# Optimization experiments

Hardware: AMD Instinct MI355X
Metric: run time of the kernel (lower is better)

Reference implementation:

```python
import jax, jax.numpy as jnp
import numpy as np

TEMPERATURE = 0.5
EPS = 1e-12  # matches torch F.normalize eps


def _l2_normalize(x):
    norm = jnp.linalg.norm(x, axis=-1, keepdims=True)
    return x / jnp.maximum(norm, EPS)


def setup_inputs() -> dict:
    key = jax.random.key(0)
    k1, k2, k3 = jax.random.split(key, 3)
    N, D = 16384, 128
    self_predictions = jax.random.normal(k1, (N, D), dtype=jnp.float32)
    pos_predictions = jax.random.normal(k2, (N, D), dtype=jnp.float32)
    labels1 = jax.random.randint(k3, (N,), 0, 100, dtype=jnp.int64)
    return {
        "self_predictions": self_predictions,
        "pos_predictions": pos_predictions,
        "labels1": labels1,
    }


def reference(self_predictions, pos_predictions, labels1):
    N = labels1.shape[0]
    a = _l2_normalize(self_predictions)  # [N, D]
    b = _l2_normalize(pos_predictions)   # [N, D]
    # cosine similarity of already-normalized rows == dot product (GEMM form)
    sim = jnp.einsum("nd,md->nm", a, b)  # [N, N]
    neg_mask = (labels1[:, None] != labels1[None, :]).astype(sim.dtype)  # 1 - mask
    neg = jnp.exp(-sim / TEMPERATURE) * neg_mask
    return neg.sum() / (N * (N - 1))
```

## Files before the change

kernel.cpp:

```cpp
#include <hip/hip_runtime.h>

typedef unsigned char u8;
typedef unsigned short u16;
typedef float f32x4 __attribute__((ext_vector_type(4)));
typedef int i32x4 __attribute__((ext_vector_type(4)));
typedef int i32x8 __attribute__((ext_vector_type(8)));

#define NROWS 16384
#define DIM 128

#define NEG2LOG2E -2.8853900817779268f
#define SCALE ((float)(1.0 / (16384.0 * 16383.0)))

#define SCALE1 0x7F7F7F7F

#define KMAX 320
#define NCORR 100
#define NGEMM 4096

__global__ __launch_bounds__(256) void norm_kernel(
    const float* __restrict__ a, const float* __restrict__ b,
    u8* __restrict__ aO, u8* __restrict__ bO)
{
    int tid  = threadIdx.x;
    int lane = tid & 63;
    int w    = tid >> 6;
    int half = lane >> 5;
    int l32  = lane & 31;
    long row = (long)blockIdx.x * 8 + w * 2 + half;

    const float4 va = ((const float4*)(a + row * DIM))[l32];
    float sa = va.x * va.x + va.y * va.y + va.z * va.z + va.w * va.w;
    #pragma unroll
    for (int off = 16; off; off >>= 1) sa += __shfl_xor(sa, off, 64);
    float inva = 1.0f / fmaxf(sqrtf(sa), 1e-12f);
    int pa = __builtin_amdgcn_cvt_pk_fp8_f32(va.x * inva, va.y * inva, 0, false);
    pa = __builtin_amdgcn_cvt_pk_fp8_f32(va.z * inva, va.w * inva, pa, true);
    ((int*)(aO + row * DIM))[l32] = pa;

    const float4 vb = ((const float4*)(b + row * DIM))[l32];
    float sb = vb.x * vb.x + vb.y * vb.y + vb.z * vb.z + vb.w * vb.w;
    #pragma unroll
    for (int off = 16; off; off >>= 1) sb += __shfl_xor(sb, off, 64);
    float invb = NEG2LOG2E / fmaxf(sqrtf(sb), 1e-12f);
    int pb = __builtin_amdgcn_cvt_pk_fp8_f32(vb.x * invb, vb.y * invb, 0, false);
    pb = __builtin_amdgcn_cvt_pk_fp8_f32(vb.z * invb, vb.w * invb, pb, true);
    ((int*)(bO + row * DIM))[l32] = pb;
}

__global__ __launch_bounds__(256, 3) void gemm_kernel(
    const u8* __restrict__ A, const u8* __restrict__ B,
    const int* __restrict__ labels,
    float* __restrict__ partials, float* __restrict__ corrP)
{
    __shared__ u8 sStage[4][2][4096];
    __shared__ int sIdx[KMAX];
    __shared__ float redS[4];
    __shared__ int sCnt;

    int tid  = threadIdx.x;
    int lane = tid & 63;
    int w    = tid >> 6;
    int mrow = lane & 15;
    int q    = lane >> 4;

    if (blockIdx.x < NCORR) {
        int l = blockIdx.x;
        if (tid == 0) sCnt = 0;
        __syncthreads();

        for (int i = tid; i < NROWS; i += 256)
            if (labels[i] == l) {
                int p = atomicAdd(&sCnt, 1);
                if (p < KMAX) sIdx[p] = i;
            }
        __syncthreads();

        int k = sCnt < KMAX ? sCnt : KMAX;
        int nt = (k + 15) >> 4;
        int ntk = nt << 4;
        for (int r = k + tid; r < ntk; r += 256) sIdx[r] = sIdx[0];
        __syncthreads();

        int npairs = nt * nt;
        float s = 0.0f;
        for (int tp = w; tp < npairs; tp += 8) {
            int tpB = tp + 4;
            bool has2 = tpB < npairs;
            int tp2 = has2 ? tpB : tp;

            int ti1 = tp / nt,  tj1 = tp  - ti1 * nt;
            int ti2 = tp2 / nt, tj2 = tp2 - ti2 * nt;
            int ri1 = sIdx[ti1 * 16 + mrow], rj1 = sIdx[tj1 * 16 + mrow];
            int ri2 = sIdx[ti2 * 16 + mrow], rj2 = sIdx[tj2 * 16 + mrow];

            const u8* pa1 = A + (size_t)ri1 * DIM + q * 32;
            const u8* pb1 = B + (size_t)rj1 * DIM + q * 32;
            const u8* pa2 = A + (size_t)ri2 * DIM + q * 32;
            const u8* pb2 = B + (size_t)rj2 * DIM + q * 32;

            i32x8 aF1, bF1, aF2, bF2;
            *((i32x4*)&aF1)     = *(const i32x4*)pa1;
            *((i32x4*)&aF1 + 1) = *(const i32x4*)(pa1 + 16);
            *((i32x4*)&bF1)     = *(const i32x4*)pb1;
            *((i32x4*)&bF1 + 1) = *(const i32x4*)(pb1 + 16);
            *((i32x4*)&aF2)     = *(const i32x4*)pa2;
            *((i32x4*)&aF2 + 1) = *(const i32x4*)(pa2 + 16);
            *((i32x4*)&bF2)     = *(const i32x4*)pb2;
            *((i32x4*)&bF2 + 1) = *(const i32x4*)(pb2 + 16);

            f32x4 acc1 = (f32x4){0.f, 0.f, 0.f, 0.f};
            f32x4 acc2 = (f32x4){0.f, 0.f, 0.f, 0.f};
            acc1 = __builtin_amdgcn_mfma_scale_f32_16x16x128_f8f6f4(
                aF1, bF1, acc1, 0, 0, 0, SCALE1, 0, SCALE1);
            acc2 = __builtin_amdgcn_mfma_scale_f32_16x16x128_f8f6f4(
                aF2, bF2, acc2, 0, 0, 0, SCALE1, 0, SCALE1);

            int i1 = ti1 * 16 + q * 4, j1 = tj1 * 16 + mrow;
            int i2 = ti2 * 16 + q * 4, j2 = tj2 * 16 + mrow;
            #pragma unroll
            for (int r = 0; r < 4; r++) {
                float e1 = __builtin_amdgcn_exp2f(acc1[r]);
                s += ((i1 + r) < k && j1 < k) ? e1 : 0.0f;
                float e2 = __builtin_amdgcn_exp2f(acc2[r]);
                s += (has2 && (i2 + r) < k && j2 < k) ? e2 : 0.0f;
            }
        }

        #pragma unroll
        for (int off = 32; off; off >>= 1) s += __shfl_xor(s, off, 64);
        if (lane == 0) redS[w] = s;
        __syncthreads();
        if (tid == 0)
            corrP[l] = (redS[0] + redS[1] + redS[2] + redS[3]) * SCALE;
        return;
    }

    int g  = blockIdx.x - NCORR;
    int r0 = (g & 255) * 64;
    int c0 = (g >> 8) * 1024 + w * 256;

    i32x8 a8[4];
    #pragma unroll
    for (int mi = 0; mi < 4; mi++) {
        const u8* pa = A + (size_t)(r0 + mi * 16 + mrow) * DIM + q * 32;
        *((i32x4*)&a8[mi])     = *(const i32x4*)pa;
        *((i32x4*)&a8[mi] + 1) = *(const i32x4*)(pa + 16);
    }

    int laneSrc = (lane >> 3) * DIM + (((lane & 7) ^ ((lane >> 3) & 7)) << 4);
    const u8* gBw = B + (size_t)c0 * DIM + laneSrc;
    u8* myStage = &sStage[w][0][0];

#define STAGE(ct, buf) do {                                                   \
        const u8* gp_ = gBw + (size_t)(ct) * (32 * DIM);                      \
        u8* lp_ = myStage + (buf) * 4096;                                     \
        _Pragma("unroll")                                                     \
        for (int i_ = 0; i_ < 4; i_++) {                                      \
            __builtin_amdgcn_global_load_lds(                                 \
                (const __attribute__((address_space(1))) void*)(gp_ + i_ * 1024), \
                (__attribute__((address_space(3))) void*)(lp_ + i_ * 1024),   \
                16, 0, 0);                                                    \
        } } while (0)

    STAGE(0, 0);

    int bOff[2];
    #pragma unroll
    for (int ni = 0; ni < 2; ni++) {
        int n = ni * 16 + mrow;
        bOff[ni] = n * DIM + (((q << 1) ^ (n & 7)) << 4);
    }

    const f32x4 z4 = (f32x4){0.f, 0.f, 0.f, 0.f};
    float s0 = 0.0f, s1 = 0.0f, s2 = 0.0f, s3 = 0.0f;

    #pragma unroll
    for (int ct = 0; ct < 8; ct++) {
        if (ct < 7) {
            STAGE(ct + 1, (ct + 1) & 1);
            asm volatile("s_waitcnt vmcnt(4)" ::: "memory");
        } else {
            asm volatile("s_waitcnt vmcnt(0)" ::: "memory");
        }
        __builtin_amdgcn_sched_barrier(0);

        const u8* sb = myStage + (ct & 1) * 4096;
        i32x8 b8[2];
        #pragma unroll
        for (int ni = 0; ni < 2; ni++) {
            *((i32x4*)&b8[ni])     = *(const i32x4*)(sb + bOff[ni]);
            *((i32x4*)&b8[ni] + 1) = *(const i32x4*)(sb + (bOff[ni] ^ 16));
        }

        f32x4 acc[4][2];
        __builtin_amdgcn_s_setprio(1);
        #pragma unroll
        for (int mi = 0; mi < 4; mi++)
            #pragma unroll
            for (int ni = 0; ni < 2; ni++)
                acc[mi][ni] = __builtin_amdgcn_mfma_scale_f32_16x16x128_f8f6f4(
                    a8[mi], b8[ni], z4, 0, 0, 0, SCALE1, 0, SCALE1);
        __builtin_amdgcn_s_setprio(0);

        #pragma unroll
        for (int mi = 0; mi < 4; mi++)
            #pragma unroll
            for (int ni = 0; ni < 2; ni++) {
                s0 += __builtin_amdgcn_exp2f(acc[mi][ni][0]);
                s1 += __builtin_amdgcn_exp2f(acc[mi][ni][1]);
                s2 += __builtin_amdgcn_exp2f(acc[mi][ni][2]);
                s3 += __builtin_amdgcn_exp2f(acc[mi][ni][3]);
            }
    }
#undef STAGE

    float s = (s0 + s1) + (s2 + s3);
    #pragma unroll
    for (int off = 32; off; off >>= 1) s += __shfl_xor(s, off, 64);

    if (lane == 0) redS[w] = s;
    __syncthreads();
    if (tid == 0) {
        float t = (redS[0] + redS[1]) + (redS[2] + redS[3]);
        partials[g] = t * SCALE;
    }
}

__global__ __launch_bounds__(256) void reduce_kernel(
    const float* __restrict__ gP, const float* __restrict__ cP,
    float* __restrict__ out)
{
    int tid = threadIdx.x;
    const float4* p4 = (const float4*)gP;
    float s = 0.0f;
    #pragma unroll 4
    for (int i = tid; i < 1024; i += 256) {
        float4 v = p4[i];
        s += (v.x + v.y) + (v.z + v.w);
    }
    if (tid < NCORR) s -= cP[tid];
    #pragma unroll
    for (int off = 32; off; off >>= 1) s += __shfl_xor(s, off, 64);
    __shared__ float red[4];
    if ((tid & 63) == 0) red[tid >> 6] = s;
    __syncthreads();
    if (tid == 0) out[0] = (red[0] + red[1]) + (red[2] + red[3]);
}

extern "C" void kernel_launch(void* const* d_in, const int* in_sizes, int n_in,
                              void* d_out, int out_size, void* d_ws, size_t ws_size,
                              hipStream_t stream) {
    const float* self_p = (const float*)d_in[0];
    const float* pos_p  = (const float*)d_in[1];
    const int*   labels = (const int*)d_in[2];
    float* out = (float*)d_out;

    u8* aB = (u8*)d_ws;
    u8* bB = aB + (size_t)NROWS * DIM;
    float* gemmP = (float*)(bB + (size_t)NROWS * DIM);
    float* corrP = gemmP + NGEMM;

    norm_kernel<<<NROWS / 8, 256, 0, stream>>>(self_p, pos_p, aB, bB);
    gemm_kernel<<<NCORR + NGEMM, 256, 0, stream>>>(aB, bB, labels, gemmP, corrP);
    reduce_kernel<<<1, 256, 0, stream>>>(gemmP, corrP, out);
}
```

Measured before the change: 121.0 us.

## Software-pipeline MFMA of next tile with exp2 of previous tile

Restructures the per-wave tile loop so the MFMAs for tile i+1 go into one accumulator set while exp2 and summation run on the other set from tile i. A sched_group_barrier pattern interleaves one MFMA with eight VALU ops. Prefetch now stages two tiles ahead before the loop starts. The aim is to hide transcendental/VALU latency behind the matrix units, at the cost of a second accumulator set (more registers) and removal of the setprio hints.

```diff
diff --git a/kernel.cpp b/kernel.cpp
--- a/kernel.cpp
+++ b/kernel.cpp
@@ -163,8 +163,6 @@
                 16, 0, 0);                                                    \
         } } while (0)
 
-    STAGE(0, 0);
-
     int bOff[2];
     #pragma unroll
     for (int ni = 0; ni < 2; ni++) {
@@ -172,48 +170,82 @@
         bOff[ni] = n * DIM + (((q << 1) ^ (n & 7)) << 4);
     }
 
+#define READB8(B8, BUF) do {                                                  \
+        const u8* sb_ = myStage + (BUF) * 4096;                               \
+        _Pragma("unroll")                                                     \
+        for (int ni_ = 0; ni_ < 2; ni_++) {                                   \
+            *((i32x4*)&(B8)[ni_])     = *(const i32x4*)(sb_ + bOff[ni_]);     \
+            *((i32x4*)&(B8)[ni_] + 1) = *(const i32x4*)(sb_ + (bOff[ni_] ^ 16)); \
+        } } while (0)
+
+#define MFMA8(ACC, B8) do {                                                   \
+        _Pragma("unroll")                                                     \
+        for (int mi_ = 0; mi_ < 4; mi_++)                                     \
+            _Pragma("unroll")                                                 \
+            for (int ni_ = 0; ni_ < 2; ni_++)                                 \
+                (ACC)[mi_][ni_] = __builtin_amdgcn_mfma_scale_f32_16x16x128_f8f6f4( \
+                    a8[mi_], (B8)[ni_], z4, 0, 0, 0, SCALE1, 0, SCALE1);      \
+        } while (0)
+
+#define EXP32(ACC) do {                                                       \
+        _Pragma("unroll")                                                     \
+        for (int mi_ = 0; mi_ < 4; mi_++)                                     \
+            _Pragma("unroll")                                                 \
+            for (int ni_ = 0; ni_ < 2; ni_++) {                               \
+                s0 += __builtin_amdgcn_exp2f((ACC)[mi_][ni_][0]);             \
+                s1 += __builtin_amdgcn_exp2f((ACC)[mi_][ni_][1]);             \
+                s2 += __builtin_amdgcn_exp2f((ACC)[mi_][ni_][2]);             \
+                s3 += __builtin_amdgcn_exp2f((ACC)[mi_][ni_][3]);             \
+            } } while (0)
+
+#define SGB_INTERLEAVE() do {                                                 \
+        _Pragma("unroll")                                                     \
+        for (int k_ = 0; k_ < 8; k_++) {                                      \
+            __builtin_amdgcn_sched_group_barrier(0x8, 1, 0);                  \
+            __builtin_amdgcn_sched_group_barrier(0x2, 8, 0);                  \
+        } } while (0)
+
+    STAGE(0, 0);
+    STAGE(1, 1);
+
     const f32x4 z4 = (f32x4){0.f, 0.f, 0.f, 0.f};
     float s0 = 0.0f, s1 = 0.0f, s2 = 0.0f, s3 = 0.0f;
 
-    #pragma unroll
-    for (int ct = 0; ct < 8; ct++) {
-        if (ct < 7) {
-            STAGE(ct + 1, (ct + 1) & 1);
+    f32x4 accA[4][2], accB[4][2];
+    i32x8 b8[2];
+
+    asm volatile("s_waitcnt vmcnt(4)" ::: "memory");
+    __builtin_amdgcn_sched_barrier(0);
+    READB8(b8, 0);
+    asm volatile("s_waitcnt lgkmcnt(0)" ::: "memory");
+    __builtin_amdgcn_sched_barrier(0);
+    MFMA8(accA, b8);
+
+    #pragma unroll
+    for (int i = 0; i < 7; ++i) {
+        if (i < 6) {
+            STAGE(i + 2, i & 1);
             asm volatile("s_waitcnt vmcnt(4)" ::: "memory");
         } else {
             asm volatile("s_waitcnt vmcnt(0)" ::: "memory");
         }
         __builtin_amdgcn_sched_barrier(0);
 
-        const u8* sb = myStage + (ct & 1) * 4096;
-        i32x8 b8[2];
-        #pragma unroll
-        for (int ni = 0; ni < 2; ni++) {
-            *((i32x4*)&b8[ni])     = *(const i32x4*)(sb + bOff[ni]);
-            *((i32x4*)&b8[ni] + 1) = *(const i32x4*)(sb + (bOff[ni] ^ 16));
-        }
-
-        f32x4 acc[4][2];
-        __builtin_amdgcn_s_setprio(1);
-        #pragma unroll
-        for (int mi = 0; mi < 4; mi++)
-            #pragma unroll
-            for (int ni = 0; ni < 2; ni++)
-                acc[mi][ni] = __builtin_amdgcn_mfma_scale_f32_16x16x128_f8f6f4(
-                    a8[mi], b8[ni], z4, 0, 0, 0, SCALE1, 0, SCALE1);
-        __builtin_amdgcn_s_setprio(0);
-
-        #pragma unroll
-        for (int mi = 0; mi < 4; mi++)
-            #pragma unroll
-            for (int ni = 0; ni < 2; ni++) {
-                s0 += __builtin_amdgcn_exp2f(acc[mi][ni][0]);
-                s1 += __builtin_amdgcn_exp2f(acc[mi][ni][1]);
-                s2 += __builtin_amdgcn_exp2f(acc[mi][ni][2]);
-                s3 += __builtin_amdgcn_exp2f(acc[mi][ni][3]);
-            }
-    }
+        READB8(b8, (i + 1) & 1);
+        asm volatile("s_waitcnt lgkmcnt(0)" ::: "memory");
+        __builtin_amdgcn_sched_barrier(0);
+
+        if ((i & 1) == 0) { MFMA8(accB, b8); EXP32(accA); }
+        else              { MFMA8(accA, b8); EXP32(accB); }
+        SGB_INTERLEAVE();
+    }
+    EXP32(accB);
+
 #undef STAGE
+#undef READB8
+#undef MFMA8
+#undef EXP32
+#undef SGB_INTERLEAVE
 
     float s = (s0 + s1) + (s2 + s3);
     #pragma unroll
```

Result: no change. 121.3 us (+0.3%).
